# Optimization experiments

Measured on AMD Instinct MI355X. Metric: run time of the kernel, lower is better.

Reference implementation:

```python
import jax, jax.numpy as jnp
import numpy as np

ODE_STEPS = 4
LN_EPS = 1e-5


def setup_inputs() -> dict:
    key = jax.random.key(0)
    ks = jax.random.split(key, 18)
    B, L, F, E, H, OH = 256, 1024, 64, 128, 128, 128
    s = lambda n: 1.0 / np.sqrt(n)
    u = lambda k, shp, n: jax.random.uniform(k, shp, jnp.float32, -s(n), s(n))
    return {
        "x": jax.random.normal(ks[0], (B, L, F), jnp.float32),
        "dt": jax.random.uniform(ks[1], (B, L), jnp.float32),
        "mask": jax.random.randint(ks[2], (B, L), 0, 2).astype(jnp.int32),
        # x_proj
        "Wx": u(ks[3], (E, F), F), "bx": u(ks[4], (E,), F),
        # ODEFunc: Linear(H,OH) -> tanh -> Linear(OH,H)
        "W1": u(ks[5], (OH, H), H), "b1": u(ks[6], (OH,), H),
        "W2": u(ks[7], (H, OH), OH), "b2": u(ks[8], (H,), OH),
        # GRUCell
        "W_ih": u(ks[9], (3 * H, E), H), "b_ih": u(ks[10], (3 * H,), H),
        "W_hh": u(ks[11], (3 * H, H), H), "b_hh": u(ks[12], (3 * H,), H),
        # head: LayerNorm + Linear(H,1)
        "ln_g": jnp.ones((H,), jnp.float32), "ln_b": jnp.zeros((H,), jnp.float32),
        "Wh": u(ks[13], (1, H), H), "bh": u(ks[14], (1,), H),
    }


def reference(x, dt, Wx, bx, W1, b1, W2, b2, W_ih, b_ih, W_hh, b_hh,
              ln_g, ln_b, Wh, bh, mask):
    B, L, F = x.shape
    H = W_hh.shape[1]

    def odefunc(h):
        return jnp.tanh(h @ W1.T + b1) @ W2.T + b2

    def ode_euler(h, dte):  # dte: [B]
        step = dte / float(ODE_STEPS)
        for _ in range(ODE_STEPS):
            h = h + step[:, None] * odefunc(h)
        return h

    def gru_cell(xe, h):
        gi = xe @ W_ih.T + b_ih
        gh = h @ W_hh.T + b_hh
        i_r, i_z, i_n = jnp.split(gi, 3, axis=-1)
        h_r, h_z, h_n = jnp.split(gh, 3, axis=-1)
        r = jax.nn.sigmoid(i_r + h_r)
        z = jax.nn.sigmoid(i_z + h_z)
        n = jnp.tanh(i_n + r * h_n)
        return (1.0 - z) * n + z * h

    def step(h, inp):
        xi, dti, mi = inp  # [B,F], [B], [B] int
        mi_f = mi.astype(x.dtype)
        active = jnp.sum(mi_f) > 0  # torch skips step only if ALL masked
        hi = ode_euler(h, dti * mi_f)
        xe = jax.nn.relu(xi @ Wx.T + bx)
        hg = gru_cell(xe, hi)
        h_new = jnp.where(active, hg, h)
        return h_new, h_new

    h0 = jnp.zeros((B, H), x.dtype)
    xs = (jnp.swapaxes(x, 0, 1), dt.T, mask.T)
    _, Hs = jax.lax.scan(step, h0, xs)       # [L,B,H]
    Hs = jnp.swapaxes(Hs, 0, 1)              # [B,L,H]

    mu = jnp.mean(Hs, axis=-1, keepdims=True)
    var = jnp.var(Hs, axis=-1, keepdims=True)
    hn = (Hs - mu) / jnp.sqrt(var + LN_EPS) * ln_g + ln_b
    logits_t = (hn @ Wh.T + bh)[..., 0]      # [B,L]

    mask_f = mask.astype(x.dtype)
    logits_t = logits_t * mask_f
    len_valid = jnp.maximum(jnp.sum(mask_f, axis=1), 1.0)
    return jnp.sum(logits_t, axis=1) / len_valid
```

## Files before the change

kernel.cpp:

```cpp
#include <hip/hip_runtime.h>

#define Bb 256
#define Ll 1024
#define Ff 64
#define Ee 128
#define Hh 128
#define CH 32

typedef _Float16 h2v __attribute__((ext_vector_type(2)));

__device__ __forceinline__ unsigned pack_h2(float a, float b) {
  h2v v; v[0] = (_Float16)a; v[1] = (_Float16)b;
  return __builtin_bit_cast(unsigned, v);
}
__device__ __forceinline__ float dot2(unsigned w, unsigned x, float acc) {
#if defined(__has_builtin) && __has_builtin(__builtin_amdgcn_fdot2)
  return __builtin_amdgcn_fdot2(__builtin_bit_cast(h2v, w),
                                __builtin_bit_cast(h2v, x), acc, false);
#else
  h2v wv = __builtin_bit_cast(h2v, w), xv = __builtin_bit_cast(h2v, x);
  acc = fmaf((float)wv[0], (float)xv[0], acc);
  return fmaf((float)wv[1], (float)xv[1], acc);
#endif
}
__device__ __forceinline__ float dppadd1(float v) {
  int s = __builtin_amdgcn_mov_dpp(__builtin_bit_cast(int, v), 0xB1, 0xF, 0xF, true);
  return v + __builtin_bit_cast(float, s);
}
__device__ __forceinline__ float dppadd2(float v) {
  int s = __builtin_amdgcn_mov_dpp(__builtin_bit_cast(int, v), 0x4E, 0xF, 0xF, true);
  return v + __builtin_bit_cast(float, s);
}
__device__ __forceinline__ float qsum(float a0, float a1) {
  return dppadd2(dppadd1(a0 + a1));
}
__device__ __forceinline__ float fast_tanh(float x) {
  float e = __expf(2.0f * x);
  return 1.0f - 2.0f / (e + 1.0f);
}
__device__ __forceinline__ float fast_sigmoid(float x) {
  return 1.0f / (1.0f + __expf(-x));
}

__device__ __forceinline__ float mv16(const unsigned* __restrict__ w,
                                      const unsigned* __restrict__ v, int q0) {
  float a0 = 0.0f, a1 = 0.0f;
#pragma unroll
  for (int c = 0; c < 4; ++c) {
    const uint4 hv = *(const uint4*)&v[q0 + 4 * c];
    a0 = dot2(w[4*c+0], hv.x, a0); a1 = dot2(w[4*c+1], hv.y, a1);
    a0 = dot2(w[4*c+2], hv.z, a0); a1 = dot2(w[4*c+3], hv.w, a1);
  }
  return qsum(a0, a1);
}
__device__ __forceinline__ float gi_gate(const unsigned* __restrict__ wrow,
                                         const unsigned* __restrict__ xe,
                                         int q0, int swi) {
  float g0 = 0.0f, g1 = 0.0f;
#pragma unroll
  for (int c = 0; c < 4; ++c) {
    const uint4 xv = *(const uint4*)&xe[q0 + 4 * c];
    const uint4 w4 = *(const uint4*)&wrow[(q0 + 4 * c) ^ swi];
    g0 = dot2(w4.x, xv.x, g0); g1 = dot2(w4.y, xv.y, g1);
    g0 = dot2(w4.z, xv.z, g0); g1 = dot2(w4.w, xv.w, g1);
  }
  return qsum(g0, g1);
}

__global__ __launch_bounds__(512, 1) void k_fused(
    const float* __restrict__ x, const float* __restrict__ dtp,
    const int* __restrict__ mask,
    const float* __restrict__ Wx, const float* __restrict__ bx,
    const float* __restrict__ W1, const float* __restrict__ b1,
    const float* __restrict__ W2, const float* __restrict__ b2,
    const float* __restrict__ Wih, const float* __restrict__ bih,
    const float* __restrict__ Whh, const float* __restrict__ bhh,
    const float* __restrict__ lng, const float* __restrict__ lnb,
    const float* __restrict__ Whd, const float* __restrict__ bhp,
    float* __restrict__ out)
{
  const int b = blockIdx.x;
  const int tid = threadIdx.x;
  const int lane = tid & 63;
  const int wv = tid >> 6;
  const int jl = lane >> 2;
  const int ks = lane & 3;
  const int j = (wv << 4) + jl;
  const int q0 = ks << 4;
  const int q0x = ks << 3;
  const int swi = (j & 15) << 2;
  const int swx = (j & 7) << 2;

  __shared__ int act_lds[Ll];
  __shared__ __align__(16) unsigned wih_lds[3 * Hh * 64];
  __shared__ __align__(16) unsigned wx_lds[Hh * 32];
  __shared__ __align__(16) unsigned x16[CH * 32];
  __shared__ __align__(16) unsigned xe16[Ee / 2];
  __shared__ __align__(16) unsigned u16[Hh / 2];
  __shared__ __align__(16) unsigned h16[2][Hh / 2];
  __shared__ float bias_lds[6 * Hh];
  __shared__ float dt_ch[CH];
  __shared__ int   m_ch[CH];
  __shared__ float red_lds[48];
  __shared__ float cc_lds[2];

  for (int t0 = tid; t0 < Ll; t0 += 512) {
    int a = 0;
#pragma unroll 8
    for (int bb = 0; bb < Bb; ++bb) a |= mask[(size_t)bb * Ll + t0];
    act_lds[t0] = a;
  }
  for (int idx = tid; idx < 3 * Hh * 64; idx += 512) {
    const int r = idx >> 6, w = idx & 63;
    wih_lds[(r << 6) | (w ^ ((r & 15) << 2))] =
        pack_h2(Wih[(size_t)r * Ee + 2 * w], Wih[(size_t)r * Ee + 2 * w + 1]);
  }
  for (int idx = tid; idx < Hh * 32; idx += 512) {
    const int r = idx >> 5, w = idx & 31;
    wx_lds[(r << 5) | (w ^ ((r & 7) << 2))] =
        pack_h2(Wx[(size_t)r * Ff + 2 * w], Wx[(size_t)r * Ff + 2 * w + 1]);
  }
  for (int i = tid; i < 3 * Hh; i += 512) {
    bias_lds[i] = bih[i];
    bias_lds[3 * Hh + i] = bhh[i];
  }
  if (tid == 0) {
    float s1 = 0.0f, s0 = 0.0f;
    for (int i = 0; i < Hh; ++i) { s1 += lng[i] * Whd[i]; s0 += lnb[i] * Whd[i]; }
    cc_lds[0] = s1; cc_lds[1] = s0 + bhp[0];
  }
  unsigned w1h[16], w2h[16], whr[16], whz[16], whn[16];
#pragma unroll
  for (int ii = 0; ii < 8; ++ii) {
    float4 a4;
    a4 = *(const float4*)&W1[(size_t)j * Hh + (ks << 5) + 4 * ii];
    w1h[2*ii] = pack_h2(a4.x, a4.y); w1h[2*ii+1] = pack_h2(a4.z, a4.w);
    a4 = *(const float4*)&W2[(size_t)j * Hh + (ks << 5) + 4 * ii];
    w2h[2*ii] = pack_h2(a4.x, a4.y); w2h[2*ii+1] = pack_h2(a4.z, a4.w);
    a4 = *(const float4*)&Whh[(size_t)j * Hh + (ks << 5) + 4 * ii];
    whr[2*ii] = pack_h2(a4.x, a4.y); whr[2*ii+1] = pack_h2(a4.z, a4.w);
    a4 = *(const float4*)&Whh[(size_t)(Hh + j) * Hh + (ks << 5) + 4 * ii];
    whz[2*ii] = pack_h2(a4.x, a4.y); whz[2*ii+1] = pack_h2(a4.z, a4.w);
    a4 = *(const float4*)&Whh[(size_t)(2 * Hh + j) * Hh + (ks << 5) + 4 * ii];
    whn[2*ii] = pack_h2(a4.x, a4.y); whn[2*ii+1] = pack_h2(a4.z, a4.w);
  }
  const float bxj = bx[j];
  const float b1j = b1[j], b2j = b2[j];
  const float gw = lng[j] * Whd[j];

  if (tid < Hh / 2) { h16[0][tid] = 0u; h16[1][tid] = 0u; }
  float hreg = 0.0f, gir = 0.0f, giz = 0.0f, gin = 0.0f;
  float acc = 0.0f, cnt = 0.0f;
  int pp = 0;
  __syncthreads();

#pragma unroll 1
  for (int t = 0; t < Ll; ++t) {
    const int tc = t & (CH - 1);
    if (tc == 0) {
      const int st = tid >> 4, g = tid & 15;
      const float4 a = *(const float4*)(x + ((size_t)b * Ll + t + st) * Ff + g * 4);
      uint2 pk; pk.x = pack_h2(a.x, a.y); pk.y = pack_h2(a.z, a.w);
      *(uint2*)&x16[st * 32 + g * 2] = pk;
      if (tid < CH) dt_ch[tid] = dtp[(size_t)b * Ll + t + tid];
      else if (tid < 2 * CH) m_ch[tid - CH] = mask[(size_t)b * Ll + t + (tid - CH)];
      __syncthreads();
    }
    const float dtv = dt_ch[tc];
    const int m = m_ch[tc];
    const int act = act_lds[t];
    const float stepv = dtv * (float)m * 0.25f;
    unsigned* hcur = h16[pp];

    {
      float p0 = 0.0f, p1 = 0.0f;
      const unsigned* xr = &x16[tc * 32];
      const unsigned* wxr = &wx_lds[j << 5];
#pragma unroll
      for (int c = 0; c < 2; ++c) {
        const uint4 xv = *(const uint4*)&xr[q0x + 4 * c];
        const uint4 w4 = *(const uint4*)&wxr[(q0x + 4 * c) ^ swx];
        p0 = dot2(w4.x, xv.x, p0); p1 = dot2(w4.y, xv.y, p1);
        p0 = dot2(w4.z, xv.z, p0); p1 = dot2(w4.w, xv.w, p1);
      }
      const float xev = fmaxf(qsum(p0, p1) + bxj, 0.0f);
      if (ks == 0) ((_Float16*)xe16)[j] = (_Float16)xev;

      const float uu = fast_tanh(mv16(w1h, hcur, q0) + b1j);
      if (ks == 0) ((_Float16*)u16)[j] = (_Float16)uu;
    }
    __syncthreads();

    {
      hreg = fmaf(stepv, mv16(w2h, u16, q0) + b2j, hreg);
      if (ks == 0) ((_Float16*)hcur)[j] = (_Float16)hreg;
      gir = gi_gate(&wih_lds[j << 6], xe16, q0, swi) + bias_lds[j];
    }
    __syncthreads();

    {
      const float uu = fast_tanh(mv16(w1h, hcur, q0) + b1j);
      if (ks == 0) ((_Float16*)u16)[j] = (_Float16)uu;
      giz = gi_gate(&wih_lds[(Hh + j) << 6], xe16, q0, swi) + bias_lds[Hh + j];
    }
    __syncthreads();
    {
      hreg = fmaf(stepv, mv16(w2h, u16, q0) + b2j, hreg);
      if (ks == 0) ((_Float16*)hcur)[j] = (_Float16)hreg;
      gin = gi_gate(&wih_lds[(2 * Hh + j) << 6], xe16, q0, swi) + bias_lds[2 * Hh + j];
    }
    __syncthreads();

#pragma unroll
    for (int s = 2; s < 4; ++s) {
      {
        const float uu = fast_tanh(mv16(w1h, hcur, q0) + b1j);
        if (ks == 0) ((_Float16*)u16)[j] = (_Float16)uu;
      }
      __syncthreads();
      {
        hreg = fmaf(stepv, mv16(w2h, u16, q0) + b2j, hreg);
        if (ks == 0) ((_Float16*)hcur)[j] = (_Float16)hreg;
      }
      __syncthreads();
    }

    {
      float pr = 0.0f, pz = 0.0f, pn = 0.0f;
#pragma unroll
      for (int c = 0; c < 4; ++c) {
        const uint4 hv = *(const uint4*)&hcur[q0 + 4 * c];
        pr = dot2(whr[4*c+0], hv.x, pr); pr = dot2(whr[4*c+1], hv.y, pr);
        pr = dot2(whr[4*c+2], hv.z, pr); pr = dot2(whr[4*c+3], hv.w, pr);
        pz = dot2(whz[4*c+0], hv.x, pz); pz = dot2(whz[4*c+1], hv.y, pz);
        pz = dot2(whz[4*c+2], hv.z, pz); pz = dot2(whz[4*c+3], hv.w, pz);
        pn = dot2(whn[4*c+0], hv.x, pn); pn = dot2(whn[4*c+1], hv.y, pn);
        pn = dot2(whn[4*c+2], hv.z, pn); pn = dot2(whn[4*c+3], hv.w, pn);
      }
      pr = qsum(pr, 0.0f) + bias_lds[3 * Hh + j];
      pz = qsum(pz, 0.0f) + bias_lds[4 * Hh + j];
      pn = qsum(pn, 0.0f) + bias_lds[5 * Hh + j];
      const float r = fast_sigmoid(gir + pr);
      const float z = fast_sigmoid(giz + pz);
      const float n = fast_tanh(gin + r * pn);
      const float hg = (1.0f - z) * n + z * hreg;
      if (act) hreg = hg;
      if (ks == 0) ((_Float16*)h16[pp ^ 1])[j] = (_Float16)hreg;

      float s1 = hreg, s2 = hreg * hreg, sd = hreg * gw;
#pragma unroll
      for (int o = 4; o <= 16; o <<= 1) {
        s1 += __shfl_xor(s1, o); s2 += __shfl_xor(s2, o); sd += __shfl_xor(sd, o);
      }
      if ((lane & 31) == 0) {
        const int slot = (wv << 1) | (lane >> 5);
        red_lds[slot * 3 + 0] = s1; red_lds[slot * 3 + 1] = s2; red_lds[slot * 3 + 2] = sd;
      }
    }
    __syncthreads();

    if (tid == 0 && m) {
      float S1 = 0.0f, S2 = 0.0f, SD = 0.0f;
#pragma unroll
      for (int q = 0; q < 16; ++q) {
        S1 += red_lds[q * 3 + 0]; S2 += red_lds[q * 3 + 1]; SD += red_lds[q * 3 + 2];
      }
      const float mu = S1 * (1.0f / 128.0f);
      const float var = S2 * (1.0f / 128.0f) - mu * mu;
      const float rstd = rsqrtf(var + 1e-5f);
      acc += rstd * (SD - mu * cc_lds[0]) + cc_lds[1];
      cnt += 1.0f;
    }
    pp ^= 1;
  }

  if (tid == 0) out[b] = acc / fmaxf(cnt, 1.0f);
}

extern "C" void kernel_launch(void* const* d_in, const int* in_sizes, int n_in,
                              void* d_out, int out_size, void* d_ws, size_t ws_size,
                              hipStream_t stream) {
  const float* x    = (const float*)d_in[0];
  const float* dt   = (const float*)d_in[1];
  const int*   mask = (const int*)d_in[2];
  const float* Wx   = (const float*)d_in[3];
  const float* bx   = (const float*)d_in[4];
  const float* W1   = (const float*)d_in[5];
  const float* b1   = (const float*)d_in[6];
  const float* W2   = (const float*)d_in[7];
  const float* b2   = (const float*)d_in[8];
  const float* Wih  = (const float*)d_in[9];
  const float* bih  = (const float*)d_in[10];
  const float* Whh  = (const float*)d_in[11];
  const float* bhh  = (const float*)d_in[12];
  const float* lng  = (const float*)d_in[13];
  const float* lnb  = (const float*)d_in[14];
  const float* Wh   = (const float*)d_in[15];
  const float* bh   = (const float*)d_in[16];
  float* out = (float*)d_out;

  k_fused<<<dim3(Bb), dim3(512), 0, stream>>>(
      x, dt, mask, Wx, bx, W1, b1, W2, b2, Wih, bih, Whh, bhh,
      lng, lnb, Wh, bh, out);
}
```

Baseline: 3.312 ms.

## Split each hidden unit across eight lanes with 1024-thread blocks

Doubles the block to 1024 threads so each hidden output is computed by eight lanes of eight packed-half words instead of four lanes of sixteen. Per-thread dot-product chains and register weights shrink, and the lane reduction gains a cross-row shuffle step. The serial LayerNorm/head reduction on thread 0 is replaced by a wave-parallel shuffle reduction, rotated across waves by timestep, with the per-wave partial sums combined at the end. The cost is more waves taking part in every block barrier, of which there are many per timestep, plus the extra shuffle in each reduction.

```diff
diff --git a/kernel.cpp b/kernel.cpp
--- a/kernel.cpp
+++ b/kernel.cpp
@@ -31,8 +31,9 @@
   int s = __builtin_amdgcn_mov_dpp(__builtin_bit_cast(int, v), 0x4E, 0xF, 0xF, true);
   return v + __builtin_bit_cast(float, s);
 }
-__device__ __forceinline__ float qsum(float a0, float a1) {
-  return dppadd2(dppadd1(a0 + a1));
+__device__ __forceinline__ float qsum8(float a0, float a1) {
+  float v = dppadd2(dppadd1(a0 + a1));
+  return v + __shfl_xor(v, 4);
 }
 __device__ __forceinline__ float fast_tanh(float x) {
   float e = __expf(2.0f * x);
@@ -42,32 +43,33 @@
   return 1.0f / (1.0f + __expf(-x));
 }
 
-__device__ __forceinline__ float mv16(const unsigned* __restrict__ w,
-                                      const unsigned* __restrict__ v, int q0) {
+__device__ __forceinline__ float mv8(const unsigned* __restrict__ w,
+                                     const unsigned* __restrict__ v, int q0) {
+  const uint4 h0 = *(const uint4*)&v[q0];
+  const uint4 h1 = *(const uint4*)&v[q0 + 4];
   float a0 = 0.0f, a1 = 0.0f;
-#pragma unroll
-  for (int c = 0; c < 4; ++c) {
-    const uint4 hv = *(const uint4*)&v[q0 + 4 * c];
-    a0 = dot2(w[4*c+0], hv.x, a0); a1 = dot2(w[4*c+1], hv.y, a1);
-    a0 = dot2(w[4*c+2], hv.z, a0); a1 = dot2(w[4*c+3], hv.w, a1);
-  }
-  return qsum(a0, a1);
-}
-__device__ __forceinline__ float gi_gate(const unsigned* __restrict__ wrow,
-                                         const unsigned* __restrict__ xe,
-                                         int q0, int swi) {
+  a0 = dot2(w[0], h0.x, a0); a1 = dot2(w[1], h0.y, a1);
+  a0 = dot2(w[2], h0.z, a0); a1 = dot2(w[3], h0.w, a1);
+  a0 = dot2(w[4], h1.x, a0); a1 = dot2(w[5], h1.y, a1);
+  a0 = dot2(w[6], h1.z, a0); a1 = dot2(w[7], h1.w, a1);
+  return qsum8(a0, a1);
+}
+__device__ __forceinline__ float gi8(const unsigned* __restrict__ wrow,
+                                     const unsigned* __restrict__ xe,
+                                     int q0, int swi) {
+  const uint4 x0 = *(const uint4*)&xe[q0];
+  const uint4 x1 = *(const uint4*)&xe[q0 + 4];
+  const uint4 w0 = *(const uint4*)&wrow[q0 ^ swi];
+  const uint4 w1 = *(const uint4*)&wrow[(q0 + 4) ^ swi];
   float g0 = 0.0f, g1 = 0.0f;
-#pragma unroll
-  for (int c = 0; c < 4; ++c) {
-    const uint4 xv = *(const uint4*)&xe[q0 + 4 * c];
-    const uint4 w4 = *(const uint4*)&wrow[(q0 + 4 * c) ^ swi];
-    g0 = dot2(w4.x, xv.x, g0); g1 = dot2(w4.y, xv.y, g1);
-    g0 = dot2(w4.z, xv.z, g0); g1 = dot2(w4.w, xv.w, g1);
-  }
-  return qsum(g0, g1);
-}
-
-__global__ __launch_bounds__(512, 1) void k_fused(
+  g0 = dot2(w0.x, x0.x, g0); g1 = dot2(w0.y, x0.y, g1);
+  g0 = dot2(w0.z, x0.z, g0); g1 = dot2(w0.w, x0.w, g1);
+  g0 = dot2(w1.x, x1.x, g0); g1 = dot2(w1.y, x1.y, g1);
+  g0 = dot2(w1.z, x1.z, g0); g1 = dot2(w1.w, x1.w, g1);
+  return qsum8(g0, g1);
+}
+
+__global__ __launch_bounds__(1024, 1) void k_fused(
     const float* __restrict__ x, const float* __restrict__ dtp,
     const int* __restrict__ mask,
     const float* __restrict__ Wx, const float* __restrict__ bx,
@@ -83,11 +85,11 @@
   const int tid = threadIdx.x;
   const int lane = tid & 63;
   const int wv = tid >> 6;
-  const int jl = lane >> 2;
-  const int ks = lane & 3;
-  const int j = (wv << 4) + jl;
-  const int q0 = ks << 4;
-  const int q0x = ks << 3;
+  const int jq = lane >> 3;
+  const int ks = lane & 7;
+  const int j = (wv << 3) + jq;
+  const int q0 = ks << 3;
+  const int q0x = ks << 2;
   const int swi = (j & 15) << 2;
   const int swx = (j & 7) << 2;
 
@@ -101,26 +103,27 @@
   __shared__ float bias_lds[6 * Hh];
   __shared__ float dt_ch[CH];
   __shared__ int   m_ch[CH];
-  __shared__ float red_lds[48];
+  __shared__ float red_lds[96];
+  __shared__ float accbuf[16], cntbuf[16];
   __shared__ float cc_lds[2];
 
-  for (int t0 = tid; t0 < Ll; t0 += 512) {
+  for (int t0 = tid; t0 < Ll; t0 += 1024) {
     int a = 0;
 #pragma unroll 8
     for (int bb = 0; bb < Bb; ++bb) a |= mask[(size_t)bb * Ll + t0];
     act_lds[t0] = a;
   }
-  for (int idx = tid; idx < 3 * Hh * 64; idx += 512) {
+  for (int idx = tid; idx < 3 * Hh * 64; idx += 1024) {
     const int r = idx >> 6, w = idx & 63;
     wih_lds[(r << 6) | (w ^ ((r & 15) << 2))] =
         pack_h2(Wih[(size_t)r * Ee + 2 * w], Wih[(size_t)r * Ee + 2 * w + 1]);
   }
-  for (int idx = tid; idx < Hh * 32; idx += 512) {
+  for (int idx = tid; idx < Hh * 32; idx += 1024) {
     const int r = idx >> 5, w = idx & 31;
     wx_lds[(r << 5) | (w ^ ((r & 7) << 2))] =
         pack_h2(Wx[(size_t)r * Ff + 2 * w], Wx[(size_t)r * Ff + 2 * w + 1]);
   }
-  for (int i = tid; i < 3 * Hh; i += 512) {
+  for (int i = tid; i < 3 * Hh; i += 1024) {
     bias_lds[i] = bih[i];
     bias_lds[3 * Hh + i] = bhh[i];
   }
@@ -129,28 +132,28 @@
     for (int i = 0; i < Hh; ++i) { s1 += lng[i] * Whd[i]; s0 += lnb[i] * Whd[i]; }
     cc_lds[0] = s1; cc_lds[1] = s0 + bhp[0];
   }
-  unsigned w1h[16], w2h[16], whr[16], whz[16], whn[16];
+  unsigned w1h[8], w2h[8], whr[8], whz[8], whn[8];
 #pragma unroll
-  for (int ii = 0; ii < 8; ++ii) {
+  for (int ii = 0; ii < 4; ++ii) {
     float4 a4;
-    a4 = *(const float4*)&W1[(size_t)j * Hh + (ks << 5) + 4 * ii];
+    a4 = *(const float4*)&W1[(size_t)j * Hh + (ks << 4) + 4 * ii];
     w1h[2*ii] = pack_h2(a4.x, a4.y); w1h[2*ii+1] = pack_h2(a4.z, a4.w);
-    a4 = *(const float4*)&W2[(size_t)j * Hh + (ks << 5) + 4 * ii];
+    a4 = *(const float4*)&W2[(size_t)j * Hh + (ks << 4) + 4 * ii];
     w2h[2*ii] = pack_h2(a4.x, a4.y); w2h[2*ii+1] = pack_h2(a4.z, a4.w);
-    a4 = *(const float4*)&Whh[(size_t)j * Hh + (ks << 5) + 4 * ii];
+    a4 = *(const float4*)&Whh[(size_t)j * Hh + (ks << 4) + 4 * ii];
     whr[2*ii] = pack_h2(a4.x, a4.y); whr[2*ii+1] = pack_h2(a4.z, a4.w);
-    a4 = *(const float4*)&Whh[(size_t)(Hh + j) * Hh + (ks << 5) + 4 * ii];
+    a4 = *(const float4*)&Whh[(size_t)(Hh + j) * Hh + (ks << 4) + 4 * ii];
     whz[2*ii] = pack_h2(a4.x, a4.y); whz[2*ii+1] = pack_h2(a4.z, a4.w);
-    a4 = *(const float4*)&Whh[(size_t)(2 * Hh + j) * Hh + (ks << 5) + 4 * ii];
+    a4 = *(const float4*)&Whh[(size_t)(2 * Hh + j) * Hh + (ks << 4) + 4 * ii];
     whn[2*ii] = pack_h2(a4.x, a4.y); whn[2*ii+1] = pack_h2(a4.z, a4.w);
   }
   const float bxj = bx[j];
   const float b1j = b1[j], b2j = b2[j];
   const float gw = lng[j] * Whd[j];
 
-  if (tid < Hh / 2) { h16[0][tid] = 0u; h16[1][tid] = 0u; }
+  if (tid < Hh) ((unsigned*)h16)[tid] = 0u;
   float hreg = 0.0f, gir = 0.0f, giz = 0.0f, gin = 0.0f;
-  float acc = 0.0f, cnt = 0.0f;
+  float accw = 0.0f, cntw = 0.0f;
   int pp = 0;
   __syncthreads();
 
@@ -158,10 +161,9 @@
   for (int t = 0; t < Ll; ++t) {
     const int tc = t & (CH - 1);
     if (tc == 0) {
-      const int st = tid >> 4, g = tid & 15;
-      const float4 a = *(const float4*)(x + ((size_t)b * Ll + t + st) * Ff + g * 4);
-      uint2 pk; pk.x = pack_h2(a.x, a.y); pk.y = pack_h2(a.z, a.w);
-      *(uint2*)&x16[st * 32 + g * 2] = pk;
+      const int st = tid >> 5, g = tid & 31;
+      const float2 a = *(const float2*)(x + ((size_t)b * Ll + t + st) * Ff + g * 2);
+      x16[st * 32 + g] = pack_h2(a.x, a.y);
       if (tid < CH) dt_ch[tid] = dtp[(size_t)b * Ll + t + tid];
       else if (tid < 2 * CH) m_ch[tid - CH] = mask[(size_t)b * Ll + t + (tid - CH)];
       __syncthreads();
@@ -173,73 +175,72 @@
     unsigned* hcur = h16[pp];
 
     {
+      const uint4 xv = *(const uint4*)&x16[tc * 32 + q0x];
+      const uint4 w4 = *(const uint4*)&wx_lds[(j << 5) + (q0x ^ swx)];
       float p0 = 0.0f, p1 = 0.0f;
-      const unsigned* xr = &x16[tc * 32];
-      const unsigned* wxr = &wx_lds[j << 5];
-#pragma unroll
-      for (int c = 0; c < 2; ++c) {
-        const uint4 xv = *(const uint4*)&xr[q0x + 4 * c];
-        const uint4 w4 = *(const uint4*)&wxr[(q0x + 4 * c) ^ swx];
-        p0 = dot2(w4.x, xv.x, p0); p1 = dot2(w4.y, xv.y, p1);
-        p0 = dot2(w4.z, xv.z, p0); p1 = dot2(w4.w, xv.w, p1);
-      }
-      const float xev = fmaxf(qsum(p0, p1) + bxj, 0.0f);
+      p0 = dot2(w4.x, xv.x, p0); p1 = dot2(w4.y, xv.y, p1);
+      p0 = dot2(w4.z, xv.z, p0); p1 = dot2(w4.w, xv.w, p1);
+      const float xev = fmaxf(qsum8(p0, p1) + bxj, 0.0f);
       if (ks == 0) ((_Float16*)xe16)[j] = (_Float16)xev;
 
-      const float uu = fast_tanh(mv16(w1h, hcur, q0) + b1j);
+      const float uu = fast_tanh(mv8(w1h, hcur, q0) + b1j);
       if (ks == 0) ((_Float16*)u16)[j] = (_Float16)uu;
     }
     __syncthreads();
 
     {
-      hreg = fmaf(stepv, mv16(w2h, u16, q0) + b2j, hreg);
+      hreg = fmaf(stepv, mv8(w2h, u16, q0) + b2j, hreg);
       if (ks == 0) ((_Float16*)hcur)[j] = (_Float16)hreg;
-      gir = gi_gate(&wih_lds[j << 6], xe16, q0, swi) + bias_lds[j];
-    }
-    __syncthreads();
-
-    {
-      const float uu = fast_tanh(mv16(w1h, hcur, q0) + b1j);
+      gir = gi8(&wih_lds[j << 6], xe16, q0, swi) + bias_lds[j];
+    }
+    __syncthreads();
+
+    {
+      const float uu = fast_tanh(mv8(w1h, hcur, q0) + b1j);
       if (ks == 0) ((_Float16*)u16)[j] = (_Float16)uu;
-      giz = gi_gate(&wih_lds[(Hh + j) << 6], xe16, q0, swi) + bias_lds[Hh + j];
-    }
-    __syncthreads();
-    {
-      hreg = fmaf(stepv, mv16(w2h, u16, q0) + b2j, hreg);
+      giz = gi8(&wih_lds[(Hh + j) << 6], xe16, q0, swi) + bias_lds[Hh + j];
+    }
+    __syncthreads();
+    {
+      hreg = fmaf(stepv, mv8(w2h, u16, q0) + b2j, hreg);
       if (ks == 0) ((_Float16*)hcur)[j] = (_Float16)hreg;
-      gin = gi_gate(&wih_lds[(2 * Hh + j) << 6], xe16, q0, swi) + bias_lds[2 * Hh + j];
+      gin = gi8(&wih_lds[(2 * Hh + j) << 6], xe16, q0, swi) + bias_lds[2 * Hh + j];
     }
     __syncthreads();
 
 #pragma unroll
     for (int s = 2; s < 4; ++s) {
       {
-        const float uu = fast_tanh(mv16(w1h, hcur, q0) + b1j);
+        const float uu = fast_tanh(mv8(w1h, hcur, q0) + b1j);
         if (ks == 0) ((_Float16*)u16)[j] = (_Float16)uu;
       }
       __syncthreads();
       {
-        hreg = fmaf(stepv, mv16(w2h, u16, q0) + b2j, hreg);
+        hreg = fmaf(stepv, mv8(w2h, u16, q0) + b2j, hreg);
         if (ks == 0) ((_Float16*)hcur)[j] = (_Float16)hreg;
       }
       __syncthreads();
     }
 
     {
+      const uint4 h0 = *(const uint4*)&hcur[q0];
+      const uint4 h1 = *(const uint4*)&hcur[q0 + 4];
       float pr = 0.0f, pz = 0.0f, pn = 0.0f;
-#pragma unroll
-      for (int c = 0; c < 4; ++c) {
-        const uint4 hv = *(const uint4*)&hcur[q0 + 4 * c];
-        pr = dot2(whr[4*c+0], hv.x, pr); pr = dot2(whr[4*c+1], hv.y, pr);
-        pr = dot2(whr[4*c+2], hv.z, pr); pr = dot2(whr[4*c+3], hv.w, pr);
-        pz = dot2(whz[4*c+0], hv.x, pz); pz = dot2(whz[4*c+1], hv.y, pz);
-        pz = dot2(whz[4*c+2], hv.z, pz); pz = dot2(whz[4*c+3], hv.w, pz);
-        pn = dot2(whn[4*c+0], hv.x, pn); pn = dot2(whn[4*c+1], hv.y, pn);
-        pn = dot2(whn[4*c+2], hv.z, pn); pn = dot2(whn[4*c+3], hv.w, pn);
-      }
-      pr = qsum(pr, 0.0f) + bias_lds[3 * Hh + j];
-      pz = qsum(pz, 0.0f) + bias_lds[4 * Hh + j];
-      pn = qsum(pn, 0.0f) + bias_lds[5 * Hh + j];
+      pr = dot2(whr[0], h0.x, pr); pr = dot2(whr[1], h0.y, pr);
+      pr = dot2(whr[2], h0.z, pr); pr = dot2(whr[3], h0.w, pr);
+      pr = dot2(whr[4], h1.x, pr); pr = dot2(whr[5], h1.y, pr);
+      pr = dot2(whr[6], h1.z, pr); pr = dot2(whr[7], h1.w, pr);
+      pz = dot2(whz[0], h0.x, pz); pz = dot2(whz[1], h0.y, pz);
+      pz = dot2(whz[2], h0.z, pz); pz = dot2(whz[3], h0.w, pz);
+      pz = dot2(whz[4], h1.x, pz); pz = dot2(whz[5], h1.y, pz);
+      pz = dot2(whz[6], h1.z, pz); pz = dot2(whz[7], h1.w, pz);
+      pn = dot2(whn[0], h0.x, pn); pn = dot2(whn[1], h0.y, pn);
+      pn = dot2(whn[2], h0.z, pn); pn = dot2(whn[3], h0.w, pn);
+      pn = dot2(whn[4], h1.x, pn); pn = dot2(whn[5], h1.y, pn);
+      pn = dot2(whn[6], h1.z, pn); pn = dot2(whn[7], h1.w, pn);
+      pr = qsum8(pr, 0.0f) + bias_lds[3 * Hh + j];
+      pz = qsum8(pz, 0.0f) + bias_lds[4 * Hh + j];
+      pn = qsum8(pn, 0.0f) + bias_lds[5 * Hh + j];
       const float r = fast_sigmoid(gir + pr);
       const float z = fast_sigmoid(giz + pz);
       const float n = fast_tanh(gin + r * pn);
@@ -248,33 +249,39 @@
       if (ks == 0) ((_Float16*)h16[pp ^ 1])[j] = (_Float16)hreg;
 
       float s1 = hreg, s2 = hreg * hreg, sd = hreg * gw;
-#pragma unroll
-      for (int o = 4; o <= 16; o <<= 1) {
-        s1 += __shfl_xor(s1, o); s2 += __shfl_xor(s2, o); sd += __shfl_xor(sd, o);
-      }
+      s1 += __shfl_xor(s1, 8);  s2 += __shfl_xor(s2, 8);  sd += __shfl_xor(sd, 8);
+      s1 += __shfl_xor(s1, 16); s2 += __shfl_xor(s2, 16); sd += __shfl_xor(sd, 16);
       if ((lane & 31) == 0) {
         const int slot = (wv << 1) | (lane >> 5);
-        red_lds[slot * 3 + 0] = s1; red_lds[slot * 3 + 1] = s2; red_lds[slot * 3 + 2] = sd;
+        red_lds[slot] = s1; red_lds[32 + slot] = s2; red_lds[64 + slot] = sd;
       }
     }
     __syncthreads();
 
-    if (tid == 0 && m) {
-      float S1 = 0.0f, S2 = 0.0f, SD = 0.0f;
+    if (wv == (t & 15) && m) {
+      float v1 = 0.0f, v2 = 0.0f, v3 = 0.0f;
+      if (lane < 32) { v1 = red_lds[lane]; v2 = red_lds[32 + lane]; v3 = red_lds[64 + lane]; }
 #pragma unroll
-      for (int q = 0; q < 16; ++q) {
-        S1 += red_lds[q * 3 + 0]; S2 += red_lds[q * 3 + 1]; SD += red_lds[q * 3 + 2];
+      for (int o = 1; o <= 16; o <<= 1) {
+        v1 += __shfl_xor(v1, o); v2 += __shfl_xor(v2, o); v3 += __shfl_xor(v3, o);
       }
-      const float mu = S1 * (1.0f / 128.0f);
-      const float var = S2 * (1.0f / 128.0f) - mu * mu;
+      const float mu = v1 * (1.0f / 128.0f);
+      const float var = v2 * (1.0f / 128.0f) - mu * mu;
       const float rstd = rsqrtf(var + 1e-5f);
-      acc += rstd * (SD - mu * cc_lds[0]) + cc_lds[1];
-      cnt += 1.0f;
+      accw += rstd * (v3 - mu * cc_lds[0]) + cc_lds[1];
+      cntw += 1.0f;
     }
     pp ^= 1;
   }
 
-  if (tid == 0) out[b] = acc / fmaxf(cnt, 1.0f);
+  if (lane == 0) { accbuf[wv] = accw; cntbuf[wv] = cntw; }
+  __syncthreads();
+  if (tid == 0) {
+    float a = 0.0f, c = 0.0f;
+#pragma unroll
+    for (int q = 0; q < 16; ++q) { a += accbuf[q]; c += cntbuf[q]; }
+    out[b] = a / fmaxf(c, 1.0f);
+  }
 }
 
 extern "C" void kernel_launch(void* const* d_in, const int* in_sizes, int n_in,
@@ -299,7 +306,7 @@
   const float* bh   = (const float*)d_in[16];
   float* out = (float*)d_out;
 
-  k_fused<<<dim3(Bb), dim3(512), 0, stream>>>(
+  k_fused<<<dim3(Bb), dim3(1024), 0, stream>>>(
       x, dt, mask, Wx, bx, W1, b1, W2, b2, Wih, bih, Whh, bhh,
       lng, lnb, Wh, bh, out);
 }
```

Result: slower. 4.125 ms (+24.5%).

## Warp-specialize block: H-waves run ODE/GRU, extra waves do input gates and LayerNorm

Applied to the files above, without the earlier changes.

Doubles the block to 1024 threads. The original 8 wavefronts handle the ODE and GRU hidden recurrence, and 8 new wavefronts compute the x projection and the input-gate matvecs, writing them to shared memory. Two of the new wavefronts also compute the previous step's LayerNorm/head reduction one step late, so that work leaves the recurrence's critical path. Wx moves into registers of the helper waves and its LDS copy is dropped. The cost is more threads per barrier, and register pressure under the 1024-thread launch bound could cause spills.

```diff
diff --git a/kernel.cpp b/kernel.cpp
--- a/kernel.cpp
+++ b/kernel.cpp
@@ -53,9 +53,9 @@
   }
   return qsum(a0, a1);
 }
-__device__ __forceinline__ float gi_gate(const unsigned* __restrict__ wrow,
-                                         const unsigned* __restrict__ xe,
-                                         int q0, int swi) {
+__device__ __forceinline__ float giq(const unsigned* __restrict__ wrow,
+                                     const unsigned* __restrict__ xe,
+                                     int q0, int swi) {
   float g0 = 0.0f, g1 = 0.0f;
 #pragma unroll
   for (int c = 0; c < 4; ++c) {
@@ -67,7 +67,7 @@
   return qsum(g0, g1);
 }
 
-__global__ __launch_bounds__(512, 1) void k_fused(
+__global__ __launch_bounds__(1024, 1) void k_fused(
     const float* __restrict__ x, const float* __restrict__ dtp,
     const int* __restrict__ mask,
     const float* __restrict__ Wx, const float* __restrict__ bx,
@@ -83,74 +83,94 @@
   const int tid = threadIdx.x;
   const int lane = tid & 63;
   const int wv = tid >> 6;
+  const bool isH = (wv < 8);
+  const int wr = wv & 7;
   const int jl = lane >> 2;
   const int ks = lane & 3;
-  const int j = (wv << 4) + jl;
+  const int j = (wr << 4) + jl;
   const int q0 = ks << 4;
   const int q0x = ks << 3;
   const int swi = (j & 15) << 2;
-  const int swx = (j & 7) << 2;
 
   __shared__ int act_lds[Ll];
   __shared__ __align__(16) unsigned wih_lds[3 * Hh * 64];
-  __shared__ __align__(16) unsigned wx_lds[Hh * 32];
   __shared__ __align__(16) unsigned x16[CH * 32];
   __shared__ __align__(16) unsigned xe16[Ee / 2];
   __shared__ __align__(16) unsigned u16[Hh / 2];
   __shared__ __align__(16) unsigned h16[2][Hh / 2];
-  __shared__ float bias_lds[6 * Hh];
+  __shared__ float gi_f[3 * Hh];
+  __shared__ float hLN[2][Hh];
+  __shared__ float bias_lds[3 * Hh];
   __shared__ float dt_ch[CH];
   __shared__ int   m_ch[CH];
-  __shared__ float red_lds[48];
+  __shared__ float lnpart[2][3];
   __shared__ float cc_lds[2];
 
-  for (int t0 = tid; t0 < Ll; t0 += 512) {
+  for (int t0 = tid; t0 < Ll; t0 += 1024) {
     int a = 0;
 #pragma unroll 8
     for (int bb = 0; bb < Bb; ++bb) a |= mask[(size_t)bb * Ll + t0];
     act_lds[t0] = a;
   }
-  for (int idx = tid; idx < 3 * Hh * 64; idx += 512) {
+  for (int idx = tid; idx < 3 * Hh * 64; idx += 1024) {
     const int r = idx >> 6, w = idx & 63;
     wih_lds[(r << 6) | (w ^ ((r & 15) << 2))] =
         pack_h2(Wih[(size_t)r * Ee + 2 * w], Wih[(size_t)r * Ee + 2 * w + 1]);
   }
-  for (int idx = tid; idx < Hh * 32; idx += 512) {
-    const int r = idx >> 5, w = idx & 31;
-    wx_lds[(r << 5) | (w ^ ((r & 7) << 2))] =
-        pack_h2(Wx[(size_t)r * Ff + 2 * w], Wx[(size_t)r * Ff + 2 * w + 1]);
-  }
-  for (int i = tid; i < 3 * Hh; i += 512) {
-    bias_lds[i] = bih[i];
-    bias_lds[3 * Hh + i] = bhh[i];
-  }
+  for (int i = tid; i < 3 * Hh; i += 1024) bias_lds[i] = bhh[i];
   if (tid == 0) {
     float s1 = 0.0f, s0 = 0.0f;
     for (int i = 0; i < Hh; ++i) { s1 += lng[i] * Whd[i]; s0 += lnb[i] * Whd[i]; }
     cc_lds[0] = s1; cc_lds[1] = s0 + bhp[0];
   }
+
   unsigned w1h[16], w2h[16], whr[16], whz[16], whn[16];
-#pragma unroll
-  for (int ii = 0; ii < 8; ++ii) {
-    float4 a4;
-    a4 = *(const float4*)&W1[(size_t)j * Hh + (ks << 5) + 4 * ii];
-    w1h[2*ii] = pack_h2(a4.x, a4.y); w1h[2*ii+1] = pack_h2(a4.z, a4.w);
-    a4 = *(const float4*)&W2[(size_t)j * Hh + (ks << 5) + 4 * ii];
-    w2h[2*ii] = pack_h2(a4.x, a4.y); w2h[2*ii+1] = pack_h2(a4.z, a4.w);
-    a4 = *(const float4*)&Whh[(size_t)j * Hh + (ks << 5) + 4 * ii];
-    whr[2*ii] = pack_h2(a4.x, a4.y); whr[2*ii+1] = pack_h2(a4.z, a4.w);
-    a4 = *(const float4*)&Whh[(size_t)(Hh + j) * Hh + (ks << 5) + 4 * ii];
-    whz[2*ii] = pack_h2(a4.x, a4.y); whz[2*ii+1] = pack_h2(a4.z, a4.w);
-    a4 = *(const float4*)&Whh[(size_t)(2 * Hh + j) * Hh + (ks << 5) + 4 * ii];
-    whn[2*ii] = pack_h2(a4.x, a4.y); whn[2*ii+1] = pack_h2(a4.z, a4.w);
-  }
-  const float bxj = bx[j];
-  const float b1j = b1[j], b2j = b2[j];
-  const float gw = lng[j] * Whd[j];
-
-  if (tid < Hh / 2) { h16[0][tid] = 0u; h16[1][tid] = 0u; }
-  float hreg = 0.0f, gir = 0.0f, giz = 0.0f, gin = 0.0f;
+  unsigned wxh[8];
+  float b1j = 0.0f, b2j = 0.0f, bxj = 0.0f;
+  float birj = 0.0f, bizj = 0.0f, binj = 0.0f;
+  if (isH) {
+#pragma unroll
+    for (int ii = 0; ii < 4; ++ii) {
+      float4 a4;
+      a4 = *(const float4*)&W1[(size_t)j * Hh + (ks << 5) + 4 * ii];
+      w1h[2*ii] = pack_h2(a4.x, a4.y); w1h[2*ii+1] = pack_h2(a4.z, a4.w);
+      a4 = *(const float4*)&W1[(size_t)j * Hh + (ks << 5) + 16 + 4 * ii];
+      w1h[8+2*ii] = pack_h2(a4.x, a4.y); w1h[8+2*ii+1] = pack_h2(a4.z, a4.w);
+      a4 = *(const float4*)&W2[(size_t)j * Hh + (ks << 5) + 4 * ii];
+      w2h[2*ii] = pack_h2(a4.x, a4.y); w2h[2*ii+1] = pack_h2(a4.z, a4.w);
+      a4 = *(const float4*)&W2[(size_t)j * Hh + (ks << 5) + 16 + 4 * ii];
+      w2h[8+2*ii] = pack_h2(a4.x, a4.y); w2h[8+2*ii+1] = pack_h2(a4.z, a4.w);
+      a4 = *(const float4*)&Whh[(size_t)j * Hh + (ks << 5) + 4 * ii];
+      whr[2*ii] = pack_h2(a4.x, a4.y); whr[2*ii+1] = pack_h2(a4.z, a4.w);
+      a4 = *(const float4*)&Whh[(size_t)j * Hh + (ks << 5) + 16 + 4 * ii];
+      whr[8+2*ii] = pack_h2(a4.x, a4.y); whr[8+2*ii+1] = pack_h2(a4.z, a4.w);
+      a4 = *(const float4*)&Whh[(size_t)(Hh + j) * Hh + (ks << 5) + 4 * ii];
+      whz[2*ii] = pack_h2(a4.x, a4.y); whz[2*ii+1] = pack_h2(a4.z, a4.w);
+      a4 = *(const float4*)&Whh[(size_t)(Hh + j) * Hh + (ks << 5) + 16 + 4 * ii];
+      whz[8+2*ii] = pack_h2(a4.x, a4.y); whz[8+2*ii+1] = pack_h2(a4.z, a4.w);
+      a4 = *(const float4*)&Whh[(size_t)(2 * Hh + j) * Hh + (ks << 5) + 4 * ii];
+      whn[2*ii] = pack_h2(a4.x, a4.y); whn[2*ii+1] = pack_h2(a4.z, a4.w);
+      a4 = *(const float4*)&Whh[(size_t)(2 * Hh + j) * Hh + (ks << 5) + 16 + 4 * ii];
+      whn[8+2*ii] = pack_h2(a4.x, a4.y); whn[8+2*ii+1] = pack_h2(a4.z, a4.w);
+    }
+    b1j = b1[j]; b2j = b2[j];
+  } else {
+#pragma unroll
+    for (int ii = 0; ii < 4; ++ii) {
+      const float4 a4 = *(const float4*)&Wx[(size_t)j * Ff + (ks << 4) + 4 * ii];
+      wxh[2*ii] = pack_h2(a4.x, a4.y); wxh[2*ii+1] = pack_h2(a4.z, a4.w);
+    }
+    bxj = bx[j];
+    birj = bih[j]; bizj = bih[Hh + j]; binj = bih[2 * Hh + j];
+  }
+  const int lidx = ((wv - 8) << 6) + lane;
+  float gw_l = 0.0f;
+  if (wv == 8 || wv == 9) gw_l = lng[lidx] * Whd[lidx];
+
+  if (tid < Hh) ((unsigned*)h16)[tid] = 0u;
+  float hreg = 0.0f;
   float acc = 0.0f, cnt = 0.0f;
+  int mprev = 0;
   int pp = 0;
   __syncthreads();
 
@@ -158,123 +178,151 @@
   for (int t = 0; t < Ll; ++t) {
     const int tc = t & (CH - 1);
     if (tc == 0) {
-      const int st = tid >> 4, g = tid & 15;
-      const float4 a = *(const float4*)(x + ((size_t)b * Ll + t + st) * Ff + g * 4);
-      uint2 pk; pk.x = pack_h2(a.x, a.y); pk.y = pack_h2(a.z, a.w);
-      *(uint2*)&x16[st * 32 + g * 2] = pk;
+      const int st = tid >> 5, g = tid & 31;
+      const float2 a = *(const float2*)(x + ((size_t)b * Ll + t + st) * Ff + g * 2);
+      x16[st * 32 + g] = pack_h2(a.x, a.y);
       if (tid < CH) dt_ch[tid] = dtp[(size_t)b * Ll + t + tid];
       else if (tid < 2 * CH) m_ch[tid - CH] = mask[(size_t)b * Ll + t + (tid - CH)];
       __syncthreads();
     }
     const float dtv = dt_ch[tc];
     const int m = m_ch[tc];
-    const int act = act_lds[t];
     const float stepv = dtv * (float)m * 0.25f;
     unsigned* hcur = h16[pp];
 
-    {
+    if (isH) {
+      const float uu = fast_tanh(mv16(w1h, hcur, q0) + b1j);
+      if (ks == 0) ((_Float16*)u16)[j] = (_Float16)uu;
+    } else {
+      const unsigned* xr = &x16[tc * 32];
       float p0 = 0.0f, p1 = 0.0f;
-      const unsigned* xr = &x16[tc * 32];
-      const unsigned* wxr = &wx_lds[j << 5];
 #pragma unroll
       for (int c = 0; c < 2; ++c) {
         const uint4 xv = *(const uint4*)&xr[q0x + 4 * c];
-        const uint4 w4 = *(const uint4*)&wxr[(q0x + 4 * c) ^ swx];
-        p0 = dot2(w4.x, xv.x, p0); p1 = dot2(w4.y, xv.y, p1);
-        p0 = dot2(w4.z, xv.z, p0); p1 = dot2(w4.w, xv.w, p1);
+        p0 = dot2(wxh[4*c+0], xv.x, p0); p1 = dot2(wxh[4*c+1], xv.y, p1);
+        p0 = dot2(wxh[4*c+2], xv.z, p0); p1 = dot2(wxh[4*c+3], xv.w, p1);
       }
       const float xev = fmaxf(qsum(p0, p1) + bxj, 0.0f);
       if (ks == 0) ((_Float16*)xe16)[j] = (_Float16)xev;
-
+    }
+    __syncthreads();
+
+    if (isH) {
+      hreg = fmaf(stepv, mv16(w2h, u16, q0) + b2j, hreg);
+      if (ks == 0) ((_Float16*)hcur)[j] = (_Float16)hreg;
+    } else {
+      const float g = giq(&wih_lds[j << 6], xe16, q0, swi) + birj;
+      if (ks == 0) gi_f[j] = g;
+    }
+    __syncthreads();
+
+    if (isH) {
       const float uu = fast_tanh(mv16(w1h, hcur, q0) + b1j);
       if (ks == 0) ((_Float16*)u16)[j] = (_Float16)uu;
-    }
-    __syncthreads();
-
-    {
+    } else {
+      const float g = giq(&wih_lds[(Hh + j) << 6], xe16, q0, swi) + bizj;
+      if (ks == 0) gi_f[Hh + j] = g;
+    }
+    __syncthreads();
+
+    if (isH) {
       hreg = fmaf(stepv, mv16(w2h, u16, q0) + b2j, hreg);
       if (ks == 0) ((_Float16*)hcur)[j] = (_Float16)hreg;
-      gir = gi_gate(&wih_lds[j << 6], xe16, q0, swi) + bias_lds[j];
-    }
-    __syncthreads();
-
-    {
+    } else {
+      const float g = giq(&wih_lds[(2 * Hh + j) << 6], xe16, q0, swi) + binj;
+      if (ks == 0) gi_f[2 * Hh + j] = g;
+    }
+    __syncthreads();
+
+    if (isH) {
       const float uu = fast_tanh(mv16(w1h, hcur, q0) + b1j);
       if (ks == 0) ((_Float16*)u16)[j] = (_Float16)uu;
-      giz = gi_gate(&wih_lds[(Hh + j) << 6], xe16, q0, swi) + bias_lds[Hh + j];
-    }
-    __syncthreads();
-    {
+    } else if (wv < 10 && t > 0) {
+      const float hv = hLN[(t & 1) ^ 1][lidx];
+      float s1 = hv, s2 = hv * hv, sd = hv * gw_l;
+#pragma unroll
+      for (int o = 1; o < 64; o <<= 1) {
+        s1 += __shfl_xor(s1, o); s2 += __shfl_xor(s2, o); sd += __shfl_xor(sd, o);
+      }
+      if (lane == 0) {
+        lnpart[wv - 8][0] = s1; lnpart[wv - 8][1] = s2; lnpart[wv - 8][2] = sd;
+      }
+    }
+    __syncthreads();
+
+    if (isH) {
       hreg = fmaf(stepv, mv16(w2h, u16, q0) + b2j, hreg);
       if (ks == 0) ((_Float16*)hcur)[j] = (_Float16)hreg;
-      gin = gi_gate(&wih_lds[(2 * Hh + j) << 6], xe16, q0, swi) + bias_lds[2 * Hh + j];
-    }
-    __syncthreads();
-
-#pragma unroll
-    for (int s = 2; s < 4; ++s) {
-      {
-        const float uu = fast_tanh(mv16(w1h, hcur, q0) + b1j);
-        if (ks == 0) ((_Float16*)u16)[j] = (_Float16)uu;
-      }
-      __syncthreads();
-      {
-        hreg = fmaf(stepv, mv16(w2h, u16, q0) + b2j, hreg);
-        if (ks == 0) ((_Float16*)hcur)[j] = (_Float16)hreg;
-      }
-      __syncthreads();
-    }
-
-    {
-      float pr = 0.0f, pz = 0.0f, pn = 0.0f;
-#pragma unroll
-      for (int c = 0; c < 4; ++c) {
-        const uint4 hv = *(const uint4*)&hcur[q0 + 4 * c];
-        pr = dot2(whr[4*c+0], hv.x, pr); pr = dot2(whr[4*c+1], hv.y, pr);
-        pr = dot2(whr[4*c+2], hv.z, pr); pr = dot2(whr[4*c+3], hv.w, pr);
-        pz = dot2(whz[4*c+0], hv.x, pz); pz = dot2(whz[4*c+1], hv.y, pz);
-        pz = dot2(whz[4*c+2], hv.z, pz); pz = dot2(whz[4*c+3], hv.w, pz);
-        pn = dot2(whn[4*c+0], hv.x, pn); pn = dot2(whn[4*c+1], hv.y, pn);
-        pn = dot2(whn[4*c+2], hv.z, pn); pn = dot2(whn[4*c+3], hv.w, pn);
-      }
-      pr = qsum(pr, 0.0f) + bias_lds[3 * Hh + j];
-      pz = qsum(pz, 0.0f) + bias_lds[4 * Hh + j];
-      pn = qsum(pn, 0.0f) + bias_lds[5 * Hh + j];
-      const float r = fast_sigmoid(gir + pr);
-      const float z = fast_sigmoid(giz + pz);
-      const float n = fast_tanh(gin + r * pn);
+    } else if (tid == 512) {
+      if (t > 0 && mprev) {
+        const float S1 = lnpart[0][0] + lnpart[1][0];
+        const float S2 = lnpart[0][1] + lnpart[1][1];
+        const float SD = lnpart[0][2] + lnpart[1][2];
+        const float mu = S1 * (1.0f / 128.0f);
+        const float var = S2 * (1.0f / 128.0f) - mu * mu;
+        const float rstd = rsqrtf(var + 1e-5f);
+        acc += rstd * (SD - mu * cc_lds[0]) + cc_lds[1];
+        cnt += 1.0f;
+      }
+      mprev = m;
+    }
+    __syncthreads();
+
+    if (isH) {
+      const float uu = fast_tanh(mv16(w1h, hcur, q0) + b1j);
+      if (ks == 0) ((_Float16*)u16)[j] = (_Float16)uu;
+    }
+    __syncthreads();
+
+    if (isH) {
+      hreg = fmaf(stepv, mv16(w2h, u16, q0) + b2j, hreg);
+      if (ks == 0) ((_Float16*)hcur)[j] = (_Float16)hreg;
+    }
+    __syncthreads();
+
+    if (isH) {
+      const float pr = mv16(whr, hcur, q0) + bias_lds[j];
+      const float pz = mv16(whz, hcur, q0) + bias_lds[Hh + j];
+      const float pn = mv16(whn, hcur, q0) + bias_lds[2 * Hh + j];
+      const float r = fast_sigmoid(gi_f[j] + pr);
+      const float z = fast_sigmoid(gi_f[Hh + j] + pz);
+      const float n = fast_tanh(gi_f[2 * Hh + j] + r * pn);
       const float hg = (1.0f - z) * n + z * hreg;
-      if (act) hreg = hg;
-      if (ks == 0) ((_Float16*)h16[pp ^ 1])[j] = (_Float16)hreg;
-
-      float s1 = hreg, s2 = hreg * hreg, sd = hreg * gw;
-#pragma unroll
-      for (int o = 4; o <= 16; o <<= 1) {
-        s1 += __shfl_xor(s1, o); s2 += __shfl_xor(s2, o); sd += __shfl_xor(sd, o);
-      }
-      if ((lane & 31) == 0) {
-        const int slot = (wv << 1) | (lane >> 5);
-        red_lds[slot * 3 + 0] = s1; red_lds[slot * 3 + 1] = s2; red_lds[slot * 3 + 2] = sd;
-      }
-    }
-    __syncthreads();
-
-    if (tid == 0 && m) {
-      float S1 = 0.0f, S2 = 0.0f, SD = 0.0f;
-#pragma unroll
-      for (int q = 0; q < 16; ++q) {
-        S1 += red_lds[q * 3 + 0]; S2 += red_lds[q * 3 + 1]; SD += red_lds[q * 3 + 2];
-      }
+      if (act_lds[t]) hreg = hg;
+      if (ks == 0) {
+        ((_Float16*)h16[pp ^ 1])[j] = (_Float16)hreg;
+        hLN[t & 1][j] = hreg;
+      }
+    }
+    __syncthreads();
+    pp ^= 1;
+  }
+
+  if (wv == 8 || wv == 9) {
+    const float hv = hLN[1][lidx];
+    float s1 = hv, s2 = hv * hv, sd = hv * gw_l;
+#pragma unroll
+    for (int o = 1; o < 64; o <<= 1) {
+      s1 += __shfl_xor(s1, o); s2 += __shfl_xor(s2, o); sd += __shfl_xor(sd, o);
+    }
+    if (lane == 0) {
+      lnpart[wv - 8][0] = s1; lnpart[wv - 8][1] = s2; lnpart[wv - 8][2] = sd;
+    }
+  }
+  __syncthreads();
+  if (tid == 512) {
+    if (mprev) {
+      const float S1 = lnpart[0][0] + lnpart[1][0];
+      const float S2 = lnpart[0][1] + lnpart[1][1];
+      const float SD = lnpart[0][2] + lnpart[1][2];
       const float mu = S1 * (1.0f / 128.0f);
       const float var = S2 * (1.0f / 128.0f) - mu * mu;
       const float rstd = rsqrtf(var + 1e-5f);
       acc += rstd * (SD - mu * cc_lds[0]) + cc_lds[1];
       cnt += 1.0f;
     }
-    pp ^= 1;
-  }
-
-  if (tid == 0) out[b] = acc / fmaxf(cnt, 1.0f);
+    out[b] = acc / fmaxf(cnt, 1.0f);
+  }
 }
 
 extern "C" void kernel_launch(void* const* d_in, const int* in_sizes, int n_in,
@@ -299,7 +347,7 @@
   const float* bh   = (const float*)d_in[16];
   float* out = (float*)d_out;
 
-  k_fused<<<dim3(Bb), dim3(512), 0, stream>>>(
+  k_fused<<<dim3(Bb), dim3(1024), 0, stream>>>(
       x, dt, mask, Wx, bx, W1, b1, W2, b2, Wih, bih, Whh, bhh,
       lng, lnb, Wh, bh, out);
 }
```

Result: slower. 5.017 ms (+51.5%).
